# Kernel tuning notes

Hardware: AMD Instinct MI355X
Metric: run time of the kernel (lower is better)

Reference implementation:

```python
import jax, jax.numpy as jnp
import numpy as np

NEG_SLOPE = 0.2
EPS = 1e-16


def gat_conv(x, edge_index, W, a_src, a_dst, b, heads, out_c, concat):
    # PyG GATConv: lin (no bias) -> per-head attention logits -> self-loops ->
    # leaky_relu -> softmax over incoming edges per dst -> weighted scatter-add -> bias
    N = x.shape[0]
    loop = jnp.arange(N)
    src = jnp.concatenate([edge_index[0], loop])  # [E+N]
    dst = jnp.concatenate([edge_index[1], loop])
    h = (x @ W).reshape(N, heads, out_c)                    # [N,H,C]
    a_s = jnp.sum(h * a_src[None], axis=-1)                 # [N,H]
    a_d = jnp.sum(h * a_dst[None], axis=-1)                 # [N,H]
    e = jax.nn.leaky_relu(a_s[src] + a_d[dst], NEG_SLOPE)   # [E+N,H]
    m = jax.ops.segment_max(e, dst, num_segments=N)         # stable softmax per dst
    e = jnp.exp(e - m[dst])
    s = jax.ops.segment_sum(e, dst, num_segments=N)
    alpha = e / (s[dst] + EPS)                              # [E+N,H]
    msg = h[src] * alpha[:, :, None]                        # [E+N,H,C]
    out = jax.ops.segment_sum(msg, dst, num_segments=N)     # [N,H,C]
    out = out.reshape(N, heads * out_c) if concat else out.mean(axis=1)
    return out + b


def setup_inputs() -> dict:
    key = jax.random.key(0)
    ks = jax.random.split(key, 20)
    N, E = 50000, 800000
    IN, HID, H, OUT = 128, 32, 4, 1
    HC = H * HID  # 128
    g = lambda k, shp: jax.random.normal(k, shp, dtype=jnp.float32) * 0.05
    inp = {
        "x": jax.random.normal(ks[0], (N, IN), dtype=jnp.float32),
        "edge_index": jax.random.randint(ks[1], (2, E), 0, N, dtype=jnp.int64),
        "batch": jnp.zeros((N,), dtype=jnp.int64),
        # conv0: GATConv(128 -> 32, heads=4, concat)
        "c0_w": g(ks[2], (IN, HC)), "c0_asrc": g(ks[3], (H, HID)),
        "c0_adst": g(ks[4], (H, HID)), "c0_b": jnp.zeros((HC,), jnp.float32),
        "s0_w": g(ks[5], (HC, IN)), "s0_b": jnp.zeros((HC,), jnp.float32),
        # conv1: GATConv(128 -> 32, heads=4, concat)
        "c1_w": g(ks[6], (HC, HC)), "c1_asrc": g(ks[7], (H, HID)),
        "c1_adst": g(ks[8], (H, HID)), "c1_b": jnp.zeros((HC,), jnp.float32),
        "s1_w": g(ks[9], (HC, HC)), "s1_b": jnp.zeros((HC,), jnp.float32),
        # conv2: GATConv(128 -> 1, heads=1, concat=False)
        "c2_w": g(ks[10], (HC, OUT)), "c2_asrc": g(ks[11], (1, OUT)),
        "c2_adst": g(ks[12], (1, OUT)), "c2_b": jnp.zeros((OUT,), jnp.float32),
        "s2_w": g(ks[13], (OUT, HC)), "s2_b": jnp.zeros((OUT,), jnp.float32),
    }
    return inp


def reference(x, edge_index, batch,
              c0_w, c0_asrc, c0_adst, c0_b, s0_w, s0_b,
              c1_w, c1_asrc, c1_adst, c1_b, s1_w, s1_b,
              c2_w, c2_asrc, c2_adst, c2_b, s2_w, s2_b):
    # layer 0 (dropout is identity in eval mode)
    h = jax.nn.relu(gat_conv(x, edge_index, c0_w, c0_asrc, c0_adst, c0_b, 4, 32, True)
                    + x @ s0_w.T + s0_b)
    # layer 1
    h = jax.nn.relu(gat_conv(h, edge_index, c1_w, c1_asrc, c1_adst, c1_b, 4, 32, True)
                    + h @ s1_w.T + s1_b)
    # output layer: heads=1, concat=False (mean over heads)
    h = (gat_conv(h, edge_index, c2_w, c2_asrc, c2_adst, c2_b, 1, 1, False)
         + h @ s2_w.T + s2_b)
    return jax.nn.sigmoid(h)
```

## Files before the change

kernel.cpp:

```cpp
#include <hip/hip_runtime.h>
#include <math.h>

#define TPB 256
#define RB 128

typedef short bf16x8 __attribute__((ext_vector_type(8)));
typedef float f32x4 __attribute__((ext_vector_type(4)));

static __device__ __forceinline__ float lrelu(float x) { return x > 0.f ? x : 0.2f * x; }
static __device__ __forceinline__ unsigned short f2bf(float f) {
  unsigned u = __float_as_uint(f);
  u += 0x7fffu + ((u >> 16) & 1u);
  return (unsigned short)(u >> 16);
}
static __device__ __forceinline__ float bflo(unsigned w) { return __uint_as_float(w << 16); }
static __device__ __forceinline__ float bfhi(unsigned w) { return __uint_as_float(w & 0xffff0000u); }
static __device__ __forceinline__ bf16x8 pack8(float4 v0, float4 v1) {
  bf16x8 r;
  r[0] = (short)f2bf(v0.x);
  r[1] = (short)f2bf(v0.y);
  r[2] = (short)f2bf(v0.z);
  r[3] = (short)f2bf(v0.w);
  r[4] = (short)f2bf(v1.x);
  r[5] = (short)f2bf(v1.y);
  r[6] = (short)f2bf(v1.z);
  r[7] = (short)f2bf(v1.w);
  return r;
}

__global__ void k_hist8(const int* __restrict__ dstE, int E, int N, int* __restrict__ deg) {
  int r = blockIdx.x & 7;
  int nb = gridDim.x >> 3;
  int lo = (int)(((long)r * N) / 8), hi = (int)(((long)(r + 1) * N) / 8);
  int EN = E + N;
  for (int e = (blockIdx.x >> 3) * TPB + threadIdx.x; e < EN; e += nb * TPB) {
    int d = (e < E) ? dstE[e] : (e - E);
    d = min(max(d, 0), N - 1);
    if (d >= lo && d < hi) atomicAdd(&deg[d], 1);
  }
}

__global__ void k_scan1(const int* __restrict__ deg, int N, int* __restrict__ csum) {
  __shared__ int sm[TPB];
  int t = threadIdx.x, i = blockIdx.x * TPB + t;
  sm[t] = (i < N) ? deg[i] : 0;
  __syncthreads();
  for (int off = TPB / 2; off; off >>= 1) {
    if (t < off) sm[t] += sm[t + off];
    __syncthreads();
  }
  if (t == 0) csum[blockIdx.x] = sm[0];
}

__global__ void k_scan2(int* __restrict__ csum, int nch) {
  __shared__ int sm[TPB];
  int t = threadIdx.x;
  int v = (t < nch) ? csum[t] : 0;
  sm[t] = v;
  __syncthreads();
  for (int off = 1; off < TPB; off <<= 1) {
    int add = (t >= off) ? sm[t - off] : 0;
    __syncthreads();
    sm[t] += add;
    __syncthreads();
  }
  if (t < nch) csum[t] = (t == 0) ? 0 : sm[t - 1];
}

__global__ void k_scan3(const int* __restrict__ deg, const int* __restrict__ csum, int N, int total,
                        int* __restrict__ row_ptr, int* __restrict__ cursor) {
  __shared__ int sm[TPB];
  int b = blockIdx.x, t = threadIdx.x, i = b * TPB + t;
  int v = (i < N) ? deg[i] : 0;
  sm[t] = v;
  __syncthreads();
  for (int off = 1; off < TPB; off <<= 1) {
    int add = (t >= off) ? sm[t - off] : 0;
    __syncthreads();
    sm[t] += add;
    __syncthreads();
  }
  if (i < N) {
    int rp = csum[b] + sm[t] - v;
    row_ptr[i] = rp;
    cursor[i] = rp;
  }
  if (i == 0) row_ptr[N] = total;
}

__global__ void k_scatter8(const int* __restrict__ srcE, const int* __restrict__ dstE, int E, int N,
                           int* __restrict__ cursor, int* __restrict__ csr_src) {
  int r = blockIdx.x & 7;
  int nb = gridDim.x >> 3;
  int lo = (int)(((long)r * N) / 8), hi = (int)(((long)(r + 1) * N) / 8);
  int EN = E + N;
  for (int e = (blockIdx.x >> 3) * TPB + threadIdx.x; e < EN; e += nb * TPB) {
    int d = (e < E) ? dstE[e] : (e - E);
    d = min(max(d, 0), N - 1);
    if (d >= lo && d < hi) {
      int s = (e < E) ? srcE[e] : (e - E);
      s = min(max(s, 0), N - 1);
      int pos = atomicAdd(&cursor[d], 1);
      csr_src[pos] = s;
    }
  }
}

__global__ void k_prep_w2(const float* __restrict__ cW0, const float* __restrict__ sW0,
                          const float* __restrict__ cW1, const float* __restrict__ sW1,
                          unsigned short* __restrict__ Wb0, unsigned short* __restrict__ Wb1) {
  int j = blockIdx.x & 255;
  int which = blockIdx.x >> 8;
  int k = threadIdx.x;
  const float* cW = which ? cW1 : cW0;
  const float* sW = which ? sW1 : sW0;
  unsigned short* Wb = which ? Wb1 : Wb0;
  Wb[j * 128 + k] = f2bf((j < 128) ? cW[k * 128 + j] : sW[(j - 128) * 128 + k]);
}

template <bool F32IN>
__global__ __launch_bounds__(TPB) void k_gemm_mfma(const void* __restrict__ Xv,
                                                   const unsigned short* __restrict__ Wb,
                                                   unsigned short* __restrict__ H16,
                                                   unsigned short* __restrict__ Sk16, int NR) {
  int wid = threadIdx.x >> 6, lane = threadIdx.x & 63;
  int r0 = blockIdx.x * 64;
  int c0 = wid * 64;
  int l15 = lane & 15, lk = lane >> 4;

  f32x4 acc[4][4];
#pragma unroll
  for (int i = 0; i < 4; ++i)
#pragma unroll
    for (int j = 0; j < 4; ++j) acc[i][j] = (f32x4){0.f, 0.f, 0.f, 0.f};

#pragma unroll
  for (int ks = 0; ks < 4; ++ks) {
    bf16x8 a[4], b[4];
#pragma unroll
    for (int rt = 0; rt < 4; ++rt) {
      int row = min(r0 + rt * 16 + l15, NR - 1);
      if (F32IN) {
        const float* xp = (const float*)Xv + (size_t)row * 128 + ks * 32 + lk * 8;
        a[rt] = pack8(*(const float4*)xp, *(const float4*)(xp + 4));
      } else {
        a[rt] = *(const bf16x8*)((const unsigned short*)Xv + (size_t)row * 128 + ks * 32 + lk * 8);
      }
    }
#pragma unroll
    for (int ct = 0; ct < 4; ++ct) {
      int col = c0 + ct * 16 + l15;
      b[ct] = *(const bf16x8*)(Wb + (size_t)col * 128 + ks * 32 + lk * 8);
    }
#pragma unroll
    for (int rt = 0; rt < 4; ++rt)
#pragma unroll
      for (int ct = 0; ct < 4; ++ct)
        acc[rt][ct] = __builtin_amdgcn_mfma_f32_16x16x32_bf16(a[rt], b[ct], acc[rt][ct], 0, 0, 0);
  }

  int orow = lk * 4;
#pragma unroll
  for (int rt = 0; rt < 4; ++rt) {
#pragma unroll
    for (int ct = 0; ct < 4; ++ct) {
      int col = c0 + ct * 16 + l15;
#pragma unroll
      for (int r = 0; r < 4; ++r) {
        int row = r0 + rt * 16 + orow + r;
        if (row < NR) {
          float v = acc[rt][ct][r];
          if (col < 128)
            H16[(size_t)row * 128 + col] = f2bf(v);
          else
            Sk16[(size_t)row * 128 + (col - 128)] = f2bf(v);
        }
      }
    }
  }
}

__global__ void k_asad(const unsigned short* __restrict__ H16, const float* __restrict__ asrc,
                       const float* __restrict__ adst, float* __restrict__ a_s, float* __restrict__ a_d, int N) {
  int i = blockIdx.x * TPB + threadIdx.x;
  if (i >= N * 4) return;
  int n = i >> 2, h = i & 3;
  const uint4* hp = (const uint4*)(H16 + (size_t)n * 128 + h * 32);
  const float4* ap = (const float4*)(asrc + h * 32);
  const float4* bp = (const float4*)(adst + h * 32);
  float sa = 0.f, sd = 0.f;
#pragma unroll
  for (int q = 0; q < 4; ++q) {
    uint4 v = hp[q];
    float f0 = bflo(v.x), f1 = bfhi(v.x), f2 = bflo(v.y), f3 = bfhi(v.y);
    float f4 = bflo(v.z), f5 = bfhi(v.z), f6 = bflo(v.w), f7 = bfhi(v.w);
    float4 a0 = ap[q * 2], a1 = ap[q * 2 + 1];
    float4 b0 = bp[q * 2], b1 = bp[q * 2 + 1];
    sa += f0 * a0.x + f1 * a0.y + f2 * a0.z + f3 * a0.w + f4 * a1.x + f5 * a1.y + f6 * a1.z + f7 * a1.w;
    sd += f0 * b0.x + f1 * b0.y + f2 * b0.z + f3 * b0.w + f4 * b1.x + f5 * b1.y + f6 * b1.z + f7 * b1.w;
  }
  a_s[i] = sa;
  a_d[i] = sd;
}

template <bool BF, bool L2F>
__global__ __launch_bounds__(TPB) void k_smax_agg(
    const int* __restrict__ row_ptr, const int* __restrict__ csr_src, const float4* __restrict__ a_s4,
    const float4* __restrict__ a_d4, const unsigned short* __restrict__ H16,
    const unsigned short* __restrict__ Sk16, const float* __restrict__ cb, const float* __restrict__ sb,
    float4* __restrict__ spill, unsigned short* __restrict__ XnB, const float* __restrict__ c2w,
    const float* __restrict__ s2w, const float* __restrict__ c2as, const float* __restrict__ c2ad,
    float* __restrict__ h2, float* __restrict__ sk2, float* __restrict__ as2, float* __restrict__ ad2, int N) {
  __shared__ int s_src[4][64];
  __shared__ float s_al[4][256];
  int wid = threadIdx.x >> 6;
  int n = blockIdx.x * 4 + wid;
  if (n >= N) return;
  int lane = threadIdx.x & 63;
  int beg = row_ptr[n], end = row_ptr[n + 1];
  int deg = end - beg;
  float4 ad = a_d4[n];
  int h = lane >> 4;
  float acc0 = 0.f, acc1 = 0.f;

  if (deg <= 64) {
    int s_l = 0;
    float4 lg = make_float4(-1e30f, -1e30f, -1e30f, -1e30f);
    if (lane < deg) {
      s_l = csr_src[beg + lane];
      float4 as = a_s4[s_l];
      lg.x = lrelu(as.x + ad.x);
      lg.y = lrelu(as.y + ad.y);
      lg.z = lrelu(as.z + ad.z);
      lg.w = lrelu(as.w + ad.w);
    }
    int maxoff = (deg <= 16) ? 8 : (deg <= 32) ? 16 : 32;
    float4 mx = lg;
    for (int off = 1; off <= maxoff; off <<= 1) {
      mx.x = fmaxf(mx.x, __shfl_xor(mx.x, off));
      mx.y = fmaxf(mx.y, __shfl_xor(mx.y, off));
      mx.z = fmaxf(mx.z, __shfl_xor(mx.z, off));
      mx.w = fmaxf(mx.w, __shfl_xor(mx.w, off));
    }
    float4 pv = make_float4(0.f, 0.f, 0.f, 0.f);
    if (lane < deg) {
      pv.x = __expf(lg.x - mx.x);
      pv.y = __expf(lg.y - mx.y);
      pv.z = __expf(lg.z - mx.z);
      pv.w = __expf(lg.w - mx.w);
    }
    float4 sm = pv;
    for (int off = 1; off <= maxoff; off <<= 1) {
      sm.x += __shfl_xor(sm.x, off);
      sm.y += __shfl_xor(sm.y, off);
      sm.z += __shfl_xor(sm.z, off);
      sm.w += __shfl_xor(sm.w, off);
    }
    pv.x *= 1.f / (sm.x + 1e-16f);
    pv.y *= 1.f / (sm.y + 1e-16f);
    pv.z *= 1.f / (sm.z + 1e-16f);
    pv.w *= 1.f / (sm.w + 1e-16f);
    s_src[wid][lane] = s_l;
    *(float4*)&s_al[wid][lane * 4] = pv;
    __builtin_amdgcn_wave_barrier();

    const unsigned short* Hb = H16 + lane * 2;
    int dpad = (deg + 3) & ~3;
    for (int j = 0; j < dpad; j += 4) {
      int s0 = s_src[wid][j + 0];
      int s1 = s_src[wid][j + 1];
      int s2 = s_src[wid][j + 2];
      int s3 = s_src[wid][j + 3];
      float a0 = s_al[wid][(j + 0) * 4 + h];
      float a1 = s_al[wid][(j + 1) * 4 + h];
      float a2 = s_al[wid][(j + 2) * 4 + h];
      float a3 = s_al[wid][(j + 3) * 4 + h];
      unsigned w0 = *(const unsigned*)(Hb + (size_t)s0 * 128);
      unsigned w1 = *(const unsigned*)(Hb + (size_t)s1 * 128);
      unsigned w2 = *(const unsigned*)(Hb + (size_t)s2 * 128);
      unsigned w3 = *(const unsigned*)(Hb + (size_t)s3 * 128);
      acc0 = fmaf(a0, bflo(w0), acc0);
      acc1 = fmaf(a0, bfhi(w0), acc1);
      acc0 = fmaf(a1, bflo(w1), acc0);
      acc1 = fmaf(a1, bfhi(w1), acc1);
      acc0 = fmaf(a2, bflo(w2), acc0);
      acc1 = fmaf(a2, bfhi(w2), acc1);
      acc0 = fmaf(a3, bflo(w3), acc0);
      acc1 = fmaf(a3, bfhi(w3), acc1);
    }
  } else {
    float4 mx = make_float4(-1e30f, -1e30f, -1e30f, -1e30f);
    for (int p = beg + lane; p < end; p += 64) {
      int s = csr_src[p];
      float4 as = a_s4[s];
      float4 lg;
      lg.x = lrelu(as.x + ad.x);
      lg.y = lrelu(as.y + ad.y);
      lg.z = lrelu(as.z + ad.z);
      lg.w = lrelu(as.w + ad.w);
      spill[p] = lg;
      mx.x = fmaxf(mx.x, lg.x);
      mx.y = fmaxf(mx.y, lg.y);
      mx.z = fmaxf(mx.z, lg.z);
      mx.w = fmaxf(mx.w, lg.w);
    }
#pragma unroll
    for (int off = 32; off; off >>= 1) {
      mx.x = fmaxf(mx.x, __shfl_xor(mx.x, off));
      mx.y = fmaxf(mx.y, __shfl_xor(mx.y, off));
      mx.z = fmaxf(mx.z, __shfl_xor(mx.z, off));
      mx.w = fmaxf(mx.w, __shfl_xor(mx.w, off));
    }
    __threadfence_block();
    float4 sm = make_float4(0.f, 0.f, 0.f, 0.f);
    for (int p = beg + lane; p < end; p += 64) {
      float4 lg = spill[p];
      float4 pv;
      pv.x = __expf(lg.x - mx.x);
      pv.y = __expf(lg.y - mx.y);
      pv.z = __expf(lg.z - mx.z);
      pv.w = __expf(lg.w - mx.w);
      spill[p] = pv;
      sm.x += pv.x;
      sm.y += pv.y;
      sm.z += pv.z;
      sm.w += pv.w;
    }
#pragma unroll
    for (int off = 32; off; off >>= 1) {
      sm.x += __shfl_xor(sm.x, off);
      sm.y += __shfl_xor(sm.y, off);
      sm.z += __shfl_xor(sm.z, off);
      sm.w += __shfl_xor(sm.w, off);
    }
    float4 inv;
    inv.x = 1.f / (sm.x + 1e-16f);
    inv.y = 1.f / (sm.y + 1e-16f);
    inv.z = 1.f / (sm.z + 1e-16f);
    inv.w = 1.f / (sm.w + 1e-16f);
    __threadfence_block();
    const float* af = (const float*)spill;
    for (int p = beg; p < end; ++p) {
      int s = csr_src[p];
      float av = af[(size_t)p * 4 + h] * ((h == 0) ? inv.x : (h == 1) ? inv.y : (h == 2) ? inv.z : inv.w);
      unsigned w = *(const unsigned*)(H16 + (size_t)s * 128 + lane * 2);
      acc0 = fmaf(av, bflo(w), acc0);
      acc1 = fmaf(av, bfhi(w), acc1);
    }
  }

  int c = lane * 2;
  unsigned skw = *(const unsigned*)(Sk16 + (size_t)n * 128 + c);
  float2 cbv = *(const float2*)(cb + c);
  float2 sbv = *(const float2*)(sb + c);
  float ox = fmaxf(acc0 + cbv.x + bflo(skw) + sbv.x, 0.f);
  float oy = fmaxf(acc1 + cbv.y + bfhi(skw) + sbv.y, 0.f);
  if (BF) {
    unsigned pk = (unsigned)f2bf(ox) | ((unsigned)f2bf(oy) << 16);
    *(unsigned*)(XnB + (size_t)n * 128 + c) = pk;
  }
  if (L2F) {
    float2 wv = *(const float2*)(c2w + c);
    float2 sv = *(const float2*)(s2w + c);
    float dh = ox * wv.x + oy * wv.y;
    float ds = ox * sv.x + oy * sv.y;
#pragma unroll
    for (int off = 32; off; off >>= 1) {
      dh += __shfl_xor(dh, off);
      ds += __shfl_xor(ds, off);
    }
    if (lane == 0) {
      h2[n] = dh;
      sk2[n] = ds;
      as2[n] = dh * c2as[0];
      ad2[n] = dh * c2ad[0];
    }
  }
}

__global__ __launch_bounds__(TPB) void k_l2_smax_agg(const int* __restrict__ row_ptr, const int* __restrict__ csr_src,
                                                     const float* __restrict__ as2, const float* __restrict__ ad2,
                                                     const float* __restrict__ h2, const float* __restrict__ sk2,
                                                     const float* __restrict__ c2b, const float* __restrict__ s2b,
                                                     float* __restrict__ out, int N) {
  int n = blockIdx.x * 4 + (threadIdx.x >> 6);
  if (n >= N) return;
  int lane = threadIdx.x & 63;
  int beg = row_ptr[n], end = row_ptr[n + 1];
  int deg = end - beg;
  float ad = ad2[n];
  float num = 0.f, den = 0.f;

  if (deg <= 64) {
    float lg = -1e30f, hv = 0.f;
    if (lane < deg) {
      int s = csr_src[beg + lane];
      lg = lrelu(as2[s] + ad);
      hv = h2[s];
    }
    float mx = lg;
#pragma unroll
    for (int off = 32; off; off >>= 1) mx = fmaxf(mx, __shfl_xor(mx, off));
    float pv = (lane < deg) ? __expf(lg - mx) : 0.f;
    num = pv * hv;
    den = pv;
  } else {
    float mx = -1e30f;
    for (int p = beg + lane; p < end; p += 64) mx = fmaxf(mx, lrelu(as2[csr_src[p]] + ad));
#pragma unroll
    for (int off = 32; off; off >>= 1) mx = fmaxf(mx, __shfl_xor(mx, off));
    for (int p = beg + lane; p < end; p += 64) {
      int s = csr_src[p];
      float pv = __expf(lrelu(as2[s] + ad) - mx);
      num += pv * h2[s];
      den += pv;
    }
  }
#pragma unroll
  for (int off = 32; off; off >>= 1) {
    num += __shfl_xor(num, off);
    den += __shfl_xor(den, off);
  }
  if (lane == 0) {
    float v = num / (den + 1e-16f) + c2b[0] + sk2[n] + s2b[0];
    out[n] = 1.f / (1.f + __expf(-v));
  }
}

extern "C" void kernel_launch(void* const* d_in, const int* in_sizes, int n_in,
                              void* d_out, int out_size, void* d_ws, size_t ws_size,
                              hipStream_t stream) {
  const float* x = (const float*)d_in[0];
  const int* ei = (const int*)d_in[1];
  const float* c0_w = (const float*)d_in[3];
  const float* c0_as = (const float*)d_in[4];
  const float* c0_ad = (const float*)d_in[5];
  const float* c0_b = (const float*)d_in[6];
  const float* s0_w = (const float*)d_in[7];
  const float* s0_b = (const float*)d_in[8];
  const float* c1_w = (const float*)d_in[9];
  const float* c1_as = (const float*)d_in[10];
  const float* c1_ad = (const float*)d_in[11];
  const float* c1_b = (const float*)d_in[12];
  const float* s1_w = (const float*)d_in[13];
  const float* s1_b = (const float*)d_in[14];
  const float* c2_w = (const float*)d_in[15];
  const float* c2_as = (const float*)d_in[16];
  const float* c2_ad = (const float*)d_in[17];
  const float* c2_b = (const float*)d_in[18];
  const float* s2_w = (const float*)d_in[19];
  const float* s2_b = (const float*)d_in[20];

  const int N = in_sizes[0] / 128;
  const int E = in_sizes[1] / 2;
  const int EN = E + N;
  const int* srcE = ei;
  const int* dstE = ei + E;

  char* wp_ = (char*)d_ws;
  auto alloc = [&](size_t bytes) -> void* {
    void* r = (void*)wp_;
    wp_ += (bytes + 255) & ~(size_t)255;
    return r;
  };
  unsigned short* Xb1 = (unsigned short*)alloc((size_t)N * 128 * 2);
  unsigned short* H16 = (unsigned short*)alloc((size_t)N * 128 * 2);
  unsigned short* Sk16 = (unsigned short*)alloc((size_t)N * 128 * 2);
  float* a_s = (float*)alloc((size_t)N * 4 * 4);
  float* a_d = (float*)alloc((size_t)N * 4 * 4);
  float* spill = (float*)alloc((size_t)EN * 4 * 4);
  unsigned short* Wb0 = (unsigned short*)alloc(256 * 128 * 2);
  unsigned short* Wb1 = (unsigned short*)alloc(256 * 128 * 2);
  int* deg = (int*)alloc((size_t)N * 4);
  int* row_ptr = (int*)alloc((size_t)(N + 1) * 4);
  int* cursor = (int*)alloc((size_t)N * 4);
  int* csum = (int*)alloc(4096 * 4);
  int* csr_src = (int*)alloc((size_t)EN * 4);
  float* h2 = (float*)alloc((size_t)N * 4);
  float* sk2 = (float*)alloc((size_t)N * 4);
  float* as2 = (float*)alloc((size_t)N * 4);
  float* ad2 = (float*)alloc((size_t)N * 4);

  const int gN4 = (N * 4 + TPB - 1) / TPB;
  const int nch = (N + TPB - 1) / TPB;
  const int gGemm = (N + 63) / 64;
  const int gWave = (N + 3) / 4;

  hipMemsetAsync(deg, 0, (size_t)N * 4, stream);
  k_hist8<<<8 * RB, TPB, 0, stream>>>(dstE, E, N, deg);
  k_scan1<<<nch, TPB, 0, stream>>>(deg, N, csum);
  k_scan2<<<1, TPB, 0, stream>>>(csum, nch);
  k_scan3<<<nch, TPB, 0, stream>>>(deg, csum, N, EN, row_ptr, cursor);
  k_scatter8<<<8 * RB, TPB, 0, stream>>>(srcE, dstE, E, N, cursor, csr_src);

  k_prep_w2<<<512, 128, 0, stream>>>(c0_w, s0_w, c1_w, s1_w, Wb0, Wb1);

  k_gemm_mfma<true><<<gGemm, TPB, 0, stream>>>(x, Wb0, H16, Sk16, N);
  k_asad<<<gN4, TPB, 0, stream>>>(H16, c0_as, c0_ad, a_s, a_d, N);
  k_smax_agg<true, false><<<gWave, TPB, 0, stream>>>(row_ptr, csr_src, (const float4*)a_s, (const float4*)a_d,
                                                     H16, Sk16, c0_b, s0_b, (float4*)spill, Xb1, nullptr, nullptr,
                                                     nullptr, nullptr, nullptr, nullptr, nullptr, nullptr, N);

  k_gemm_mfma<false><<<gGemm, TPB, 0, stream>>>(Xb1, Wb1, H16, Sk16, N);
  k_asad<<<gN4, TPB, 0, stream>>>(H16, c1_as, c1_ad, a_s, a_d, N);
  k_smax_agg<false, true><<<gWave, TPB, 0, stream>>>(row_ptr, csr_src, (const float4*)a_s, (const float4*)a_d,
                                                     H16, Sk16, c1_b, s1_b, (float4*)spill, nullptr, c2_w, s2_w,
                                                     c2_as, c2_ad, h2, sk2, as2, ad2, N);

  k_l2_smax_agg<<<gWave, TPB, 0, stream>>>(row_ptr, csr_src, as2, ad2, h2, sk2, c2_b, s2_b, (float*)d_out, N);
}
```

Before: 367.6 us.

## Gather 16-byte feature rows with four edges per wave in aggregation

Restructures the softmax-aggregation kernel so each wave splits into four 16-lane groups. Each group handles a different edge and each lane loads 8 bf16 features with one 16-byte load, where before every lane loaded 4 bytes for each edge in turn. Partial sums are combined across groups with shuffles before the epilogue, which now writes 8 outputs per lane from the first group only. The goal is fewer, wider gather instructions and fewer loop iterations, at the cost of more registers, an extra cross-group reduction, and idle lanes during the store.

```diff
diff --git a/kernel.cpp b/kernel.cpp
--- a/kernel.cpp
+++ b/kernel.cpp
@@ -212,16 +212,19 @@
     const float* __restrict__ s2w, const float* __restrict__ c2as, const float* __restrict__ c2ad,
     float* __restrict__ h2, float* __restrict__ sk2, float* __restrict__ as2, float* __restrict__ ad2, int N) {
   __shared__ int s_src[4][64];
-  __shared__ float s_al[4][256];
+  __shared__ float s_al[4][64][4];
   int wid = threadIdx.x >> 6;
   int n = blockIdx.x * 4 + wid;
   if (n >= N) return;
   int lane = threadIdx.x & 63;
+  int eg = lane >> 4, cl = lane & 15;
+  int h = cl >> 2;
   int beg = row_ptr[n], end = row_ptr[n + 1];
   int deg = end - beg;
   float4 ad = a_d4[n];
-  int h = lane >> 4;
-  float acc0 = 0.f, acc1 = 0.f;
+  float acc[8];
+#pragma unroll
+  for (int i = 0; i < 8; ++i) acc[i] = 0.f;
 
   if (deg <= 64) {
     int s_l = 0;
@@ -261,32 +264,22 @@
     pv.z *= 1.f / (sm.z + 1e-16f);
     pv.w *= 1.f / (sm.w + 1e-16f);
     s_src[wid][lane] = s_l;
-    *(float4*)&s_al[wid][lane * 4] = pv;
+    *(float4*)&s_al[wid][lane][0] = pv;
     __builtin_amdgcn_wave_barrier();
 
-    const unsigned short* Hb = H16 + lane * 2;
     int dpad = (deg + 3) & ~3;
     for (int j = 0; j < dpad; j += 4) {
-      int s0 = s_src[wid][j + 0];
-      int s1 = s_src[wid][j + 1];
-      int s2 = s_src[wid][j + 2];
-      int s3 = s_src[wid][j + 3];
-      float a0 = s_al[wid][(j + 0) * 4 + h];
-      float a1 = s_al[wid][(j + 1) * 4 + h];
-      float a2 = s_al[wid][(j + 2) * 4 + h];
-      float a3 = s_al[wid][(j + 3) * 4 + h];
-      unsigned w0 = *(const unsigned*)(Hb + (size_t)s0 * 128);
-      unsigned w1 = *(const unsigned*)(Hb + (size_t)s1 * 128);
-      unsigned w2 = *(const unsigned*)(Hb + (size_t)s2 * 128);
-      unsigned w3 = *(const unsigned*)(Hb + (size_t)s3 * 128);
-      acc0 = fmaf(a0, bflo(w0), acc0);
-      acc1 = fmaf(a0, bfhi(w0), acc1);
-      acc0 = fmaf(a1, bflo(w1), acc0);
-      acc1 = fmaf(a1, bfhi(w1), acc1);
-      acc0 = fmaf(a2, bflo(w2), acc0);
-      acc1 = fmaf(a2, bfhi(w2), acc1);
-      acc0 = fmaf(a3, bflo(w3), acc0);
-      acc1 = fmaf(a3, bfhi(w3), acc1);
+      int sj = s_src[wid][j + eg];
+      float aj = s_al[wid][j + eg][h];
+      uint4 w = *(const uint4*)(H16 + (size_t)sj * 128 + cl * 8);
+      acc[0] = fmaf(aj, bflo(w.x), acc[0]);
+      acc[1] = fmaf(aj, bfhi(w.x), acc[1]);
+      acc[2] = fmaf(aj, bflo(w.y), acc[2]);
+      acc[3] = fmaf(aj, bfhi(w.y), acc[3]);
+      acc[4] = fmaf(aj, bflo(w.z), acc[4]);
+      acc[5] = fmaf(aj, bfhi(w.z), acc[5]);
+      acc[6] = fmaf(aj, bflo(w.w), acc[6]);
+      acc[7] = fmaf(aj, bfhi(w.w), acc[7]);
     }
   } else {
     float4 mx = make_float4(-1e30f, -1e30f, -1e30f, -1e30f);
@@ -333,39 +326,61 @@
       sm.z += __shfl_xor(sm.z, off);
       sm.w += __shfl_xor(sm.w, off);
     }
-    float4 inv;
-    inv.x = 1.f / (sm.x + 1e-16f);
-    inv.y = 1.f / (sm.y + 1e-16f);
-    inv.z = 1.f / (sm.z + 1e-16f);
-    inv.w = 1.f / (sm.w + 1e-16f);
+    float invh = 1.f / (((h == 0) ? sm.x : (h == 1) ? sm.y : (h == 2) ? sm.z : sm.w) + 1e-16f);
     __threadfence_block();
     const float* af = (const float*)spill;
-    for (int p = beg; p < end; ++p) {
+    for (int p = beg + eg; p < end; p += 4) {
       int s = csr_src[p];
-      float av = af[(size_t)p * 4 + h] * ((h == 0) ? inv.x : (h == 1) ? inv.y : (h == 2) ? inv.z : inv.w);
-      unsigned w = *(const unsigned*)(H16 + (size_t)s * 128 + lane * 2);
-      acc0 = fmaf(av, bflo(w), acc0);
-      acc1 = fmaf(av, bfhi(w), acc1);
-    }
-  }
-
-  int c = lane * 2;
-  unsigned skw = *(const unsigned*)(Sk16 + (size_t)n * 128 + c);
-  float2 cbv = *(const float2*)(cb + c);
-  float2 sbv = *(const float2*)(sb + c);
-  float ox = fmaxf(acc0 + cbv.x + bflo(skw) + sbv.x, 0.f);
-  float oy = fmaxf(acc1 + cbv.y + bfhi(skw) + sbv.y, 0.f);
-  if (BF) {
-    unsigned pk = (unsigned)f2bf(ox) | ((unsigned)f2bf(oy) << 16);
-    *(unsigned*)(XnB + (size_t)n * 128 + c) = pk;
+      float aj = af[(size_t)p * 4 + h] * invh;
+      uint4 w = *(const uint4*)(H16 + (size_t)s * 128 + cl * 8);
+      acc[0] = fmaf(aj, bflo(w.x), acc[0]);
+      acc[1] = fmaf(aj, bfhi(w.x), acc[1]);
+      acc[2] = fmaf(aj, bflo(w.y), acc[2]);
+      acc[3] = fmaf(aj, bfhi(w.y), acc[3]);
+      acc[4] = fmaf(aj, bflo(w.z), acc[4]);
+      acc[5] = fmaf(aj, bfhi(w.z), acc[5]);
+      acc[6] = fmaf(aj, bflo(w.w), acc[6]);
+      acc[7] = fmaf(aj, bfhi(w.w), acc[7]);
+    }
+  }
+
+#pragma unroll
+  for (int i = 0; i < 8; ++i) {
+    acc[i] += __shfl_xor(acc[i], 16);
+    acc[i] += __shfl_xor(acc[i], 32);
+  }
+
+  int c = cl * 8;
+  uint4 skw = *(const uint4*)(Sk16 + (size_t)n * 128 + c);
+  float4 cb0 = *(const float4*)(cb + c), cb1 = *(const float4*)(cb + c + 4);
+  float4 sb0 = *(const float4*)(sb + c), sb1 = *(const float4*)(sb + c + 4);
+  float o[8];
+  o[0] = fmaxf(acc[0] + cb0.x + bflo(skw.x) + sb0.x, 0.f);
+  o[1] = fmaxf(acc[1] + cb0.y + bfhi(skw.x) + sb0.y, 0.f);
+  o[2] = fmaxf(acc[2] + cb0.z + bflo(skw.y) + sb0.z, 0.f);
+  o[3] = fmaxf(acc[3] + cb0.w + bfhi(skw.y) + sb0.w, 0.f);
+  o[4] = fmaxf(acc[4] + cb1.x + bflo(skw.z) + sb1.x, 0.f);
+  o[5] = fmaxf(acc[5] + cb1.y + bfhi(skw.z) + sb1.y, 0.f);
+  o[6] = fmaxf(acc[6] + cb1.z + bflo(skw.w) + sb1.z, 0.f);
+  o[7] = fmaxf(acc[7] + cb1.w + bfhi(skw.w) + sb1.w, 0.f);
+
+  if (BF && eg == 0) {
+    uint4 pk;
+    pk.x = (unsigned)f2bf(o[0]) | ((unsigned)f2bf(o[1]) << 16);
+    pk.y = (unsigned)f2bf(o[2]) | ((unsigned)f2bf(o[3]) << 16);
+    pk.z = (unsigned)f2bf(o[4]) | ((unsigned)f2bf(o[5]) << 16);
+    pk.w = (unsigned)f2bf(o[6]) | ((unsigned)f2bf(o[7]) << 16);
+    *(uint4*)(XnB + (size_t)n * 128 + c) = pk;
   }
   if (L2F) {
-    float2 wv = *(const float2*)(c2w + c);
-    float2 sv = *(const float2*)(s2w + c);
-    float dh = ox * wv.x + oy * wv.y;
-    float ds = ox * sv.x + oy * sv.y;
-#pragma unroll
-    for (int off = 32; off; off >>= 1) {
+    float4 w0 = *(const float4*)(c2w + c), w1 = *(const float4*)(c2w + c + 4);
+    float4 v0 = *(const float4*)(s2w + c), v1 = *(const float4*)(s2w + c + 4);
+    float dh = o[0] * w0.x + o[1] * w0.y + o[2] * w0.z + o[3] * w0.w + o[4] * w1.x + o[5] * w1.y + o[6] * w1.z +
+               o[7] * w1.w;
+    float ds = o[0] * v0.x + o[1] * v0.y + o[2] * v0.z + o[3] * v0.w + o[4] * v1.x + o[5] * v1.y + o[6] * v1.z +
+               o[7] * v1.w;
+#pragma unroll
+    for (int off = 1; off <= 8; off <<= 1) {
       dh += __shfl_xor(dh, off);
       ds += __shfl_xor(ds, off);
     }
```

New measurement: 374.2 us. About the same (+1.8%).
